# Optimization experiments

Hardware: AMD Instinct MI355X
Metric: run time of the kernel (lower is better)

The kernel has to match this reference:

```python
import jax, jax.numpy as jnp
import numpy as np

B, P, C = 2, 512, 21          # images, proposals/image, classes (incl background)
REG = 5                       # xc, yc, w, h, angle(deg)
DET = 100                     # detections_per_img
IMW, IMH = 1024, 800
SCORE_THRESH = 0.05
NMS_THR = 0.5
WEIGHTS = (10.0, 10.0, 5.0, 5.0, 3.0)
BBOX_XFORM_CLIP = float(np.log(1000.0 / 16.0))
MAXV = 8                      # max vertices of quad-quad intersection


def setup_inputs() -> dict:
    key = jax.random.key(0)
    k1, k2, k3 = jax.random.split(key, 3)
    class_logits = jax.random.normal(k1, (B * P, C), jnp.float32)
    box_regression = jax.random.normal(k2, (B * P, C * REG), jnp.float32)
    u = jax.random.uniform(k3, (B * P, 5), jnp.float32)
    rrects = jnp.stack([
        u[:, 0] * IMW,            # xc
        u[:, 1] * IMH,            # yc
        u[:, 2] * 200.0 + 16.0,   # w
        u[:, 3] * 200.0 + 16.0,   # h
        u[:, 4] * 360.0 - 180.0,  # angle in degrees
    ], axis=1)
    return {"class_logits": class_logits, "box_regression": box_regression, "rrects": rrects}


def rect_pts(r):
    # r [..., 5] -> corner points [..., 4, 2] (CCW quad in math coords)
    xc, yc, w, h, ang = (r[..., i] for i in range(5))
    t = ang * (jnp.pi / 180.0)
    c, s = jnp.cos(t), jnp.sin(t)
    dx, dy = w * 0.5, h * 0.5
    ox = jnp.stack([-dx, dx, dx, -dx], -1)
    oy = jnp.stack([-dy, -dy, dy, dy], -1)
    x = xc[..., None] + c[..., None] * ox - s[..., None] * oy
    y = yc[..., None] + s[..., None] * ox + c[..., None] * oy
    return jnp.stack([x, y], -1)


def decode(deltas, anchors):
    # BoxCoder.decode for rotated boxes, weights (wx,wy,ww,wh,wa)
    d = deltas.reshape(-1, C, REG) / jnp.asarray(WEIGHTS, deltas.dtype)
    dx, dy, dw, dh, da = (d[..., i] for i in range(REG))
    dw = jnp.minimum(dw, BBOX_XFORM_CLIP)
    dh = jnp.minimum(dh, BBOX_XFORM_CLIP)
    xc, yc, w, h, a = (anchors[:, i:i + 1] for i in range(5))
    px = dx * w + xc
    py = dy * h + yc
    pw = jnp.exp(dw) * w
    ph = jnp.exp(dh) * h
    pa = da * (180.0 / jnp.pi) + a
    return jnp.stack([px, py, pw, ph, pa], -1)  # [N, C, 5]


def _clip_edge(poly, n, a, b):
    # Sutherland-Hodgman clip of convex poly (buffer [MAXV,2], count n) by halfplane left of a->b
    d = b - a
    out = jnp.zeros((MAXV, 2), poly.dtype)
    m = jnp.int32(0)
    nn = jnp.maximum(n, 1)
    for i in range(MAXV):
        act = i < n
        s = poly[i]
        e = poly[jnp.mod(i + 1, nn)]
        cs = d[0] * (s[1] - a[1]) - d[1] * (s[0] - a[0])
        ce = d[0] * (e[1] - a[1]) - d[1] * (e[0] - a[0])
        denom = cs - ce
        t = cs / jnp.where(jnp.abs(denom) > 1e-12, denom, 1e-12)
        ip = s + t * (e - s)
        s_in = cs >= 0
        e_in = ce >= 0
        app1 = act & (s_in != e_in)           # crossing -> intersection point
        out = out.at[m].set(jnp.where(app1, ip, out[m]))
        m = m + app1.astype(jnp.int32)
        app2 = act & e_in                     # end point inside -> keep it
        out = out.at[m].set(jnp.where(app2, e, out[m]))
        m = m + app2.astype(jnp.int32)
    return out, m


def inter_area(p1, p2):
    # exact intersection area of two convex quads [4,2]
    poly = jnp.zeros((MAXV, 2), p1.dtype).at[:4].set(p1)
    n = jnp.int32(4)
    for k in range(4):
        poly, n = _clip_edge(poly, n, p2[k], p2[(k + 1) % 4])
    idx = jnp.arange(MAXV)
    nn = jnp.maximum(n, 1)
    nxt = jnp.mod(idx + 1, nn)
    cross = poly[:, 0] * poly[nxt, 1] - poly[nxt, 0] * poly[:, 1]
    area = 0.5 * jnp.abs(jnp.sum(jnp.where(idx < n, cross, 0.0)))
    return jnp.where(n >= 3, area, 0.0)


def _nms_one(args):
    # greedy rotated NMS on one (image,class) score-sorted set
    rr, valid = args                       # [P,5], [P] bool (sorted by desc score)
    pts = rect_pts(rr)                     # [P,4,2]
    areas = rr[:, 2] * rr[:, 3]
    inter = jax.vmap(lambda p: jax.vmap(lambda q: inter_area(p, q))(pts))(pts)
    iou = inter / (areas[:, None] + areas[None, :] - inter + 1e-8)
    n = rr.shape[0]
    def body(i, keep):
        sup = jnp.any(keep & (iou[i] > NMS_THR))
        return keep.at[i].set(valid[i] & jnp.logical_not(sup))
    return jax.lax.fori_loop(0, n, body, jnp.zeros((n,), bool))


def reference(class_logits, box_regression, rrects):
    scores = jax.nn.softmax(class_logits, -1)           # [N,C]
    proposals = decode(box_regression, rrects)          # [N,C,5]
    pts = rect_pts(proposals)                           # [N,C,4,2]
    mn, mx = pts.min(-2), pts.max(-2)
    bb = jnp.concatenate([mn, mx], -1)                  # xyxy [N,C,4]
    bb = jnp.stack([
        jnp.clip(bb[..., 0], 0.0, IMW - 1.0),
        jnp.clip(bb[..., 1], 0.0, IMH - 1.0),
        jnp.clip(bb[..., 2], 0.0, IMW - 1.0),
        jnp.clip(bb[..., 3], 0.0, IMH - 1.0),
    ], -1)

    # per-image, foreground classes only; [B, C-1, P, ...]
    sc = scores.reshape(B, P, C)[:, :, 1:].transpose(0, 2, 1)
    pr = proposals.reshape(B, P, C, 5)[:, :, 1:].transpose(0, 2, 1, 3)
    bx = bb.reshape(B, P, C, 4)[:, :, 1:].transpose(0, 2, 1, 3)

    valid = sc > SCORE_THRESH
    masked = jnp.where(valid, sc, -1.0)
    order = jnp.argsort(-masked, axis=-1)               # desc score per class
    sc_s = jnp.take_along_axis(masked, order, -1)
    valid_s = jnp.take_along_axis(valid, order, -1)
    pr_s = jnp.take_along_axis(pr, order[..., None], 2)
    bx_s = jnp.take_along_axis(bx, order[..., None], 2)

    keep = jax.lax.map(_nms_one, (jax.lax.stop_gradient(pr_s).reshape(-1, P, 5),
                                  valid_s.reshape(-1, P))).reshape(B, C - 1, P)
    keep = jax.lax.stop_gradient(keep)

    msk = jnp.where(keep, sc_s, -1.0)
    flat_s = msk.reshape(B, -1)                         # [B,(C-1)*P]
    top_idx = jax.lax.top_k(flat_s, DET)[1]
    sel_s = jnp.take_along_axis(flat_s, top_idx, -1)
    ok = sel_s > 0.0
    sel_bb = jnp.take_along_axis(bx_s.reshape(B, -1, 4), top_idx[..., None], 1)
    sel_rr = jnp.take_along_axis(pr_s.reshape(B, -1, 5), top_idx[..., None], 1)
    lab = jnp.broadcast_to(jnp.arange(1, C, dtype=jnp.int32)[:, None], (C - 1, P)).reshape(-1)
    sel_lab = lab[top_idx]

    out_bb = jnp.where(ok[..., None], sel_bb, 0.0)
    out_rr = jnp.where(ok[..., None], sel_rr, 0.0)
    out_sc = jnp.where(ok, sel_s, 0.0)
    out_lab = jnp.where(ok, sel_lab, 0)
    return out_bb, out_rr, out_sc, out_lab
```

## Files before the change

kernel.cpp:

```cpp
#include <hip/hip_runtime.h>
#include <stdint.h>

#pragma clang fp contract(off)

#define B_ 2
#define P_ 512
#define C_ 21
#define CF 20
#define DET 100
#define SCORE_THRESH 0.05f
#define NMS_THR 0.5f
#define BBOX_CLIP 4.135166556742356f
#define NC (CF * DET)

typedef unsigned long long u64;
typedef unsigned int u32;

__device__ __forceinline__ u32 f2o(float f) {
  u32 u = __float_as_uint(f);
  return (u & 0x80000000u) ? ~u : (u | 0x80000000u);
}
__device__ __forceinline__ float o2f(u32 o) {
  u32 u = (o & 0x80000000u) ? (o ^ 0x80000000u) : ~o;
  return __uint_as_float(u);
}

__global__ void __launch_bounds__(256)
prep_kernel(const float* __restrict__ logits,
            const float* __restrict__ breg,
            const float* __restrict__ rrects,
            float* __restrict__ scsS,
            float* __restrict__ ptsS,
            float* __restrict__ aabbS,
            float* __restrict__ pr5S,
            float* __restrict__ areaS,
            int* __restrict__ gV,
            u64* __restrict__ sup) {
  int g = blockIdx.x;
  int b = g / CF, cf = g % CF, c = cf + 1;
  int tid = threadIdx.x;

  __shared__ u64 lkey[P_];
  __shared__ int cnt;
  if (tid == 0) cnt = 0;

  u64 kreg[2];
  float fx[2][4], fy[2][4];
  float fab[2][4];
  float fp5[2][5];
  float far_[2];
  float fsc[2];
  #pragma unroll
  for (int e = 0; e < 2; ++e) {
    int p = tid + e * 256;
    int n = b * P_ + p;
    const float* lg = logits + n * C_;
    float mx = lg[0];
    for (int k = 1; k < C_; ++k) mx = fmaxf(mx, lg[k]);
    float den = 0.f;
    for (int k = 0; k < C_; ++k) den += expf(lg[k] - mx);
    float sc = expf(lg[c] - mx) / den;

    const float* d = breg + n * (C_ * 5) + c * 5;
    float dx = d[0] / 10.0f, dy = d[1] / 10.0f;
    float dw = d[2] / 5.0f, dh = d[3] / 5.0f, da = d[4] / 3.0f;
    dw = fminf(dw, BBOX_CLIP);
    dh = fminf(dh, BBOX_CLIP);
    const float* an = rrects + n * 5;
    float px = dx * an[2] + an[0];
    float py = dy * an[3] + an[1];
    float pw = expf(dw) * an[2];
    float ph = expf(dh) * an[3];
    float pa = da * 57.29577951308232f + an[4];
    fp5[e][0] = px; fp5[e][1] = py; fp5[e][2] = pw; fp5[e][3] = ph; fp5[e][4] = pa;
    far_[e] = pw * ph;

    float t = pa * 0.017453292519943295f;
    float cs = cosf(t), sn = sinf(t);
    float hx = pw * 0.5f, hy = ph * 0.5f;
    float ox[4] = {-hx, hx, hx, -hx};
    float oy[4] = {-hy, -hy, hy, hy};
    float minx = 1e30f, miny = 1e30f, maxx = -1e30f, maxy = -1e30f;
    #pragma unroll
    for (int qq = 0; qq < 4; ++qq) {
      float x = px + cs * ox[qq] - sn * oy[qq];
      float y = py + sn * ox[qq] + cs * oy[qq];
      fx[e][qq] = x; fy[e][qq] = y;
      minx = fminf(minx, x); maxx = fmaxf(maxx, x);
      miny = fminf(miny, y); maxy = fmaxf(maxy, y);
    }
    fab[e][0] = minx; fab[e][1] = miny; fab[e][2] = maxx; fab[e][3] = maxy;

    bool valid = sc > SCORE_THRESH;
    float v = valid ? sc : -1.0f;
    fsc[e] = v;
    u64 key = ((u64)f2o(v) << 32) | (u32)(~(u32)p);
    lkey[p] = key;
    kreg[e] = key;
    u64 m = __ballot(valid);
    if ((tid & 63) == 0) atomicAdd(&cnt, __popcll(m));
  }
  for (int w = tid; w < P_ * 8; w += 256) sup[(size_t)g * P_ * 8 + w] = 0ull;
  __syncthreads();

  u64 k0 = kreg[0], k1 = kreg[1];
  int r0 = 0, r1 = 0;
  for (int s = 0; s < P_; ++s) {
    u64 ks = lkey[s];
    r0 += (ks > k0) ? 1 : 0;
    r1 += (ks > k1) ? 1 : 0;
  }
  #pragma unroll
  for (int e = 0; e < 2; ++e) {
    if (fsc[e] > 0.f) {
      int r = (e == 0) ? r0 : r1;
      int so = g * P_ + r;
      scsS[so] = fsc[e];
      ((float4*)ptsS)[so * 2]     = make_float4(fx[e][0], fx[e][1], fx[e][2], fx[e][3]);
      ((float4*)ptsS)[so * 2 + 1] = make_float4(fy[e][0], fy[e][1], fy[e][2], fy[e][3]);
      ((float4*)aabbS)[so] = make_float4(fab[e][0], fab[e][1], fab[e][2], fab[e][3]);
      pr5S[so * 5 + 0] = fp5[e][0]; pr5S[so * 5 + 1] = fp5[e][1];
      pr5S[so * 5 + 2] = fp5[e][2]; pr5S[so * 5 + 3] = fp5[e][3];
      pr5S[so * 5 + 4] = fp5[e][4];
      areaS[so] = far_[e];
    }
  }
  if (tid == 0) gV[g] = cnt;
}

__device__ __forceinline__ float inter_area_reg(const float qx[4], const float qy[4],
                                                const float rx[4], const float ry[4]) {
  float px_[8], py_[8];
  #pragma unroll
  for (int t = 0; t < 8; ++t) { px_[t] = (t < 4) ? qx[t] : 0.f; py_[t] = (t < 4) ? qy[t] : 0.f; }
  int n = 4;
  #pragma unroll
  for (int e = 0; e < 4; ++e) {
    float a0 = rx[e], a1 = ry[e];
    float b0 = rx[(e + 1) & 3], b1 = ry[(e + 1) & 3];
    float dx = b0 - a0, dy = b1 - a1;
    float ox_[8], oy_[8];
    #pragma unroll
    for (int t = 0; t < 8; ++t) { ox_[t] = 0.f; oy_[t] = 0.f; }
    float cr[8];
    #pragma unroll
    for (int t = 0; t < 8; ++t) cr[t] = dx * (py_[t] - a1) - dy * (px_[t] - a0);
    int m = 0;
    int nn = (n > 1) ? n : 1;
    #pragma unroll
    for (int t = 0; t < 8; ++t) {
      bool act = t < n;
      float sx = px_[t], sy = py_[t];
      float ex, ey, ce;
      if (t == 7) { ex = px_[0]; ey = py_[0]; ce = cr[0]; }
      else {
        bool wrap = (t + 1 == nn);
        ex = wrap ? px_[0] : px_[t + 1];
        ey = wrap ? py_[0] : py_[t + 1];
        ce = wrap ? cr[0] : cr[t + 1];
      }
      float cs = cr[t];
      float denom = cs - ce;
      float dn = (fabsf(denom) > 1e-12f) ? denom : 1e-12f;
      float tt = cs / dn;
      float ipx = sx + tt * (ex - sx);
      float ipy = sy + tt * (ey - sy);
      bool s_in = cs >= 0.f, e_in = ce >= 0.f;
      bool app1 = act && (s_in != e_in);
      #pragma unroll
      for (int s2 = 0; s2 < 8; ++s2) {
        bool wr = app1 && (m == s2);
        ox_[s2] = wr ? ipx : ox_[s2];
        oy_[s2] = wr ? ipy : oy_[s2];
      }
      m += app1 ? 1 : 0;
      bool app2 = act && e_in;
      #pragma unroll
      for (int s2 = 0; s2 < 8; ++s2) {
        bool wr = app2 && (m == s2);
        ox_[s2] = wr ? ex : ox_[s2];
        oy_[s2] = wr ? ey : oy_[s2];
      }
      m += app2 ? 1 : 0;
    }
    n = m;
    #pragma unroll
    for (int t = 0; t < 8; ++t) { px_[t] = ox_[t]; py_[t] = oy_[t]; }
  }
  int nn = (n > 1) ? n : 1;
  float s = 0.f;
  #pragma unroll
  for (int t = 0; t < 8; ++t) {
    if (t < n) {
      float nx_x, nx_y;
      if (t == 7) { nx_x = px_[0]; nx_y = py_[0]; }
      else {
        bool wrap = (t + 1 == nn);
        nx_x = wrap ? px_[0] : px_[t + 1];
        nx_y = wrap ? py_[0] : py_[t + 1];
      }
      s += px_[t] * nx_y - nx_x * py_[t];
    }
  }
  float area = 0.5f * fabsf(s);
  return (n >= 3) ? area : 0.f;
}

#define PPT 4
#define TPB 256
__global__ void pair_kernel(const int* __restrict__ gV,
                            const float* __restrict__ aabbS,
                            const float* __restrict__ areaS,
                            const float* __restrict__ ptsS,
                            u64* __restrict__ sup) {
  int g = blockIdx.y;
  int V = gV[g];
  int Tp = V * (V - 1) / 2;
  int base = blockIdx.x * (TPB * PPT);
  if (base >= Tp) return;
  __shared__ u32 q[TPB * PPT];
  __shared__ int qn;
  int tid = threadIdx.x;
  if (tid == 0) qn = 0;
  __syncthreads();
  const float4* ab = (const float4*)aabbS;
  for (int t = 0; t < PPT; ++t) {
    int kk = base + t * TPB + tid;
    if (kk >= Tp) break;
    float kf = (float)kk;
    int i = (int)((1.0f + sqrtf(1.0f + 8.0f * kf)) * 0.5f);
    while (i * (i - 1) / 2 > kk) --i;
    while ((i + 1) * i / 2 <= kk) ++i;
    int j = kk - i * (i - 1) / 2;
    float4 bi = ab[g * P_ + i];
    float4 bj = ab[g * P_ + j];
    bool ov = (bi.x <= bj.z) && (bj.x <= bi.z) && (bi.y <= bj.w) && (bj.y <= bi.w);
    if (ov) {
      int s = atomicAdd(&qn, 1);
      q[s] = (u32)((i << 9) | j);
    }
  }
  __syncthreads();
  int nq = qn;
  const float4* pS = (const float4*)ptsS;
  for (int s = tid; s < nq; s += TPB) {
    u32 pk = q[s];
    int i = (int)(pk >> 9), j = (int)(pk & 511);
    float4 ax = pS[(g * P_ + i) * 2];
    float4 ay = pS[(g * P_ + i) * 2 + 1];
    float4 bx = pS[(g * P_ + j) * 2];
    float4 by = pS[(g * P_ + j) * 2 + 1];
    float qx[4] = {ax.x, ax.y, ax.z, ax.w};
    float qy[4] = {ay.x, ay.y, ay.z, ay.w};
    float rx[4] = {bx.x, bx.y, bx.z, bx.w};
    float ry[4] = {by.x, by.y, by.z, by.w};
    float ai = areaS[g * P_ + i];
    float aj = areaS[g * P_ + j];
    float inter = inter_area_reg(qx, qy, rx, ry);
    float iou = inter / (((ai + aj) - inter) + 1e-8f);
    if (iou > NMS_THR)
      atomicOr(&sup[((size_t)g * P_ + i) * 8 + (j >> 6)], 1ull << (j & 63));
  }
}

__global__ void greedy_kernel(const float* __restrict__ scsS, const int* __restrict__ gV,
                              const float* __restrict__ aabbS, const float* __restrict__ pr5S,
                              const u64* __restrict__ sup,
                              u64* __restrict__ cand, float* __restrict__ rec) {
  int g = blockIdx.x;
  int tid = threadIdx.x;
  __shared__ u64 lsup[P_ * 8];
  __shared__ u32 skeep[16];
  int V = gV[g];
  for (int w = tid; w < V * 8; w += 64) lsup[w] = sup[(size_t)g * P_ * 8 + w];
  __syncthreads();
  u64 keepw = 0;
  u64 cur = (tid < 8 && V > 0) ? lsup[tid] : 0ull;
  for (int i = 0; i < V; ++i) {
    u64 nxt = (tid < 8 && (i + 1) < V) ? lsup[(i + 1) * 8 + tid] : 0ull;
    bool supd = __any((cur & keepw) != 0ull);
    if (!supd && tid == (i >> 6)) keepw |= 1ull << (i & 63);
    cur = nxt;
  }
  if (tid < 8) { skeep[tid * 2] = (u32)keepw; skeep[tid * 2 + 1] = (u32)(keepw >> 32); }
  __syncthreads();
  int cls = g % CF;
  int tot = 0;
  #pragma unroll
  for (int t = 0; t < 16; ++t) tot += __popc(skeep[t]);
  for (int r = tid; r < V; r += 64) {
    if ((skeep[r >> 5] >> (r & 31)) & 1u) {
      int slot = __popc(skeep[r >> 5] & ((1u << (r & 31)) - 1u));
      for (int t = 0; t < (r >> 5); ++t) slot += __popc(skeep[t]);
      if (slot < DET) {
        float sv = scsS[g * P_ + r];
        int flat = cls * P_ + r;
        cand[g * DET + slot] = ((u64)f2o(sv) << 32) | (u32)(~(u32)flat);
        int so = g * P_ + r;
        float* rr = rec + (size_t)(g * DET + slot) * 12;
        rr[0] = fminf(fmaxf(aabbS[so * 4 + 0], 0.f), 1023.0f);
        rr[1] = fminf(fmaxf(aabbS[so * 4 + 1], 0.f), 799.0f);
        rr[2] = fminf(fmaxf(aabbS[so * 4 + 2], 0.f), 1023.0f);
        rr[3] = fminf(fmaxf(aabbS[so * 4 + 3], 0.f), 799.0f);
        rr[4] = pr5S[so * 5 + 0]; rr[5] = pr5S[so * 5 + 1]; rr[6] = pr5S[so * 5 + 2];
        rr[7] = pr5S[so * 5 + 3]; rr[8] = pr5S[so * 5 + 4];
        rr[9] = sv;
        rr[10] = (float)(cls + 1);
        rr[11] = 0.f;
      }
    }
  }
  int fill = tot < DET ? tot : DET;
  for (int s = fill + tid; s < DET; s += 64) cand[g * DET + s] = 0ull;
}

__global__ void rank_kernel(const u64* __restrict__ cand, const float* __restrict__ rec,
                            float* __restrict__ out) {
  int b = blockIdx.y;
  int tid = threadIdx.x;
  __shared__ u64 lc[NC];
  __shared__ int ncand;
  if (tid == 0) ncand = 0;
  __syncthreads();
  int nz = 0;
  for (int i = tid; i < NC; i += 256) {
    u64 v = cand[b * NC + i];
    lc[i] = v;
    nz += (v != 0ull) ? 1 : 0;
  }
  u64 m = __ballot(nz > 0);
  if (nz > 0) atomicAdd(&ncand, nz);
  (void)m;
  __syncthreads();
  int ci = blockIdx.x * 256 + tid;
  if (ci >= NC) return;
  if (blockIdx.x == 0 && tid < DET && tid >= ncand) {
    int o_bb = (b * DET + tid) * 4;
    int o_rr = B_ * DET * 4 + (b * DET + tid) * 5;
    int o_sc = B_ * DET * 9 + b * DET + tid;
    int o_lab = B_ * DET * 10 + b * DET + tid;
    out[o_bb + 0] = 0.f; out[o_bb + 1] = 0.f; out[o_bb + 2] = 0.f; out[o_bb + 3] = 0.f;
    out[o_rr + 0] = 0.f; out[o_rr + 1] = 0.f; out[o_rr + 2] = 0.f;
    out[o_rr + 3] = 0.f; out[o_rr + 4] = 0.f;
    out[o_sc] = 0.f;
    out[o_lab] = 0.f;
  }
  u64 k = lc[ci];
  if (k == 0ull) return;
  int rank = 0;
  #pragma unroll
  for (int gp = 0; gp < CF; ++gp) {
    int lo = 0, hi = DET;
    while (lo < hi) {
      int mid = (lo + hi) >> 1;
      if (lc[gp * DET + mid] > k) lo = mid + 1; else hi = mid;
    }
    rank += lo;
  }
  if (rank >= DET) return;
  const float* rr = rec + (size_t)(b * NC + ci) * 12;
  int o_bb = (b * DET + rank) * 4;
  int o_rr = B_ * DET * 4 + (b * DET + rank) * 5;
  int o_sc = B_ * DET * 9 + b * DET + rank;
  int o_lab = B_ * DET * 10 + b * DET + rank;
  out[o_bb + 0] = rr[0]; out[o_bb + 1] = rr[1];
  out[o_bb + 2] = rr[2]; out[o_bb + 3] = rr[3];
  out[o_rr + 0] = rr[4]; out[o_rr + 1] = rr[5]; out[o_rr + 2] = rr[6];
  out[o_rr + 3] = rr[7]; out[o_rr + 4] = rr[8];
  out[o_sc] = rr[9];
  out[o_lab] = rr[10];
}

extern "C" void kernel_launch(void* const* d_in, const int* in_sizes, int n_in,
                              void* d_out, int out_size, void* d_ws, size_t ws_size,
                              hipStream_t stream) {
  const float* logits = (const float*)d_in[0];
  const float* breg   = (const float*)d_in[1];
  const float* rrects = (const float*)d_in[2];
  float* out = (float*)d_out;

  const int G = B_ * CF;
  u64*   sup  = (u64*)d_ws;
  u64*   cand = sup + (size_t)G * P_ * 8;
  int*   gV   = (int*)(cand + G * DET);
  float* scsS = (float*)(gV + 64);
  float* ptsS = scsS + (size_t)G * P_;
  float* aabbS = ptsS + (size_t)G * P_ * 8;
  float* pr5S = aabbS + (size_t)G * P_ * 4;
  float* areaS = pr5S + (size_t)G * P_ * 5;
  float* rec  = areaS + (size_t)G * P_;

  prep_kernel<<<G, 256, 0, stream>>>(logits, breg, rrects,
                                     scsS, ptsS, aabbS, pr5S, areaS, gV, sup);
  pair_kernel<<<dim3(128, G), TPB, 0, stream>>>(gV, aabbS, areaS, ptsS, sup);
  greedy_kernel<<<G, 64, 0, stream>>>(scsS, gV, aabbS, pr5S, sup, cand, rec);
  rank_kernel<<<dim3((NC + 255) / 256, B_), 256, 0, stream>>>(cand, rec, out);
}
```

Measured before the change: 133.8 us.

## Compact valid keys before ranking and use one proposal per thread in prep

The prep kernel now runs 512 threads per (image,class) group, one proposal each, instead of 256 threads handling two. Valid keys are compacted into shared memory with a ballot prefix sum, so each thread ranks itself only against the valid candidates rather than all 512, unrolled by four. The logits loads and softmax loop are fully unrolled into registers. This cuts the O(P^2) rank loop when few scores pass the threshold, at the cost of more registers per thread and an extra barrier.

```diff
diff --git a/kernel.cpp b/kernel.cpp
--- a/kernel.cpp
+++ b/kernel.cpp
@@ -25,7 +25,7 @@
   return __uint_as_float(u);
 }
 
-__global__ void __launch_bounds__(256)
+__global__ void __launch_bounds__(512)
 prep_kernel(const float* __restrict__ logits,
             const float* __restrict__ breg,
             const float* __restrict__ rrects,
@@ -39,93 +39,102 @@
   int g = blockIdx.x;
   int b = g / CF, cf = g % CF, c = cf + 1;
   int tid = threadIdx.x;
-
-  __shared__ u64 lkey[P_];
-  __shared__ int cnt;
-  if (tid == 0) cnt = 0;
-
-  u64 kreg[2];
-  float fx[2][4], fy[2][4];
-  float fab[2][4];
-  float fp5[2][5];
-  float far_[2];
-  float fsc[2];
-  #pragma unroll
-  for (int e = 0; e < 2; ++e) {
-    int p = tid + e * 256;
-    int n = b * P_ + p;
-    const float* lg = logits + n * C_;
-    float mx = lg[0];
-    for (int k = 1; k < C_; ++k) mx = fmaxf(mx, lg[k]);
-    float den = 0.f;
-    for (int k = 0; k < C_; ++k) den += expf(lg[k] - mx);
-    float sc = expf(lg[c] - mx) / den;
-
-    const float* d = breg + n * (C_ * 5) + c * 5;
-    float dx = d[0] / 10.0f, dy = d[1] / 10.0f;
-    float dw = d[2] / 5.0f, dh = d[3] / 5.0f, da = d[4] / 3.0f;
-    dw = fminf(dw, BBOX_CLIP);
-    dh = fminf(dh, BBOX_CLIP);
-    const float* an = rrects + n * 5;
-    float px = dx * an[2] + an[0];
-    float py = dy * an[3] + an[1];
-    float pw = expf(dw) * an[2];
-    float ph = expf(dh) * an[3];
-    float pa = da * 57.29577951308232f + an[4];
-    fp5[e][0] = px; fp5[e][1] = py; fp5[e][2] = pw; fp5[e][3] = ph; fp5[e][4] = pa;
-    far_[e] = pw * ph;
-
-    float t = pa * 0.017453292519943295f;
-    float cs = cosf(t), sn = sinf(t);
-    float hx = pw * 0.5f, hy = ph * 0.5f;
-    float ox[4] = {-hx, hx, hx, -hx};
-    float oy[4] = {-hy, -hy, hy, hy};
-    float minx = 1e30f, miny = 1e30f, maxx = -1e30f, maxy = -1e30f;
-    #pragma unroll
-    for (int qq = 0; qq < 4; ++qq) {
-      float x = px + cs * ox[qq] - sn * oy[qq];
-      float y = py + sn * ox[qq] + cs * oy[qq];
-      fx[e][qq] = x; fy[e][qq] = y;
-      minx = fminf(minx, x); maxx = fmaxf(maxx, x);
-      miny = fminf(miny, y); maxy = fmaxf(maxy, y);
-    }
-    fab[e][0] = minx; fab[e][1] = miny; fab[e][2] = maxx; fab[e][3] = maxy;
-
-    bool valid = sc > SCORE_THRESH;
-    float v = valid ? sc : -1.0f;
-    fsc[e] = v;
-    u64 key = ((u64)f2o(v) << 32) | (u32)(~(u32)p);
-    lkey[p] = key;
-    kreg[e] = key;
-    u64 m = __ballot(valid);
-    if ((tid & 63) == 0) atomicAdd(&cnt, __popcll(m));
-  }
-  for (int w = tid; w < P_ * 8; w += 256) sup[(size_t)g * P_ * 8 + w] = 0ull;
-  __syncthreads();
-
-  u64 k0 = kreg[0], k1 = kreg[1];
-  int r0 = 0, r1 = 0;
-  for (int s = 0; s < P_; ++s) {
-    u64 ks = lkey[s];
-    r0 += (ks > k0) ? 1 : 0;
-    r1 += (ks > k1) ? 1 : 0;
-  }
-  #pragma unroll
-  for (int e = 0; e < 2; ++e) {
-    if (fsc[e] > 0.f) {
-      int r = (e == 0) ? r0 : r1;
-      int so = g * P_ + r;
-      scsS[so] = fsc[e];
-      ((float4*)ptsS)[so * 2]     = make_float4(fx[e][0], fx[e][1], fx[e][2], fx[e][3]);
-      ((float4*)ptsS)[so * 2 + 1] = make_float4(fy[e][0], fy[e][1], fy[e][2], fy[e][3]);
-      ((float4*)aabbS)[so] = make_float4(fab[e][0], fab[e][1], fab[e][2], fab[e][3]);
-      pr5S[so * 5 + 0] = fp5[e][0]; pr5S[so * 5 + 1] = fp5[e][1];
-      pr5S[so * 5 + 2] = fp5[e][2]; pr5S[so * 5 + 3] = fp5[e][3];
-      pr5S[so * 5 + 4] = fp5[e][4];
-      areaS[so] = far_[e];
-    }
-  }
-  if (tid == 0) gV[g] = cnt;
+  int w = tid >> 6, lane = tid & 63;
+
+  __shared__ u64 ckey[P_ + 8];
+  __shared__ int wcnt[8];
+
+  int p = tid;
+  int n = b * P_ + p;
+  const float* lgp = logits + n * C_;
+  float lg[C_];
+  #pragma unroll
+  for (int k = 0; k < C_; ++k) lg[k] = lgp[k];
+  float mx = lg[0];
+  #pragma unroll
+  for (int k = 1; k < C_; ++k) mx = fmaxf(mx, lg[k]);
+  float den = 0.f, num = 0.f;
+  #pragma unroll
+  for (int k = 0; k < C_; ++k) {
+    float ex = expf(lg[k] - mx);
+    den += ex;
+    num = (k == c) ? ex : num;
+  }
+  float sc = num / den;
+
+  const float* d = breg + n * (C_ * 5) + c * 5;
+  float dx = d[0] / 10.0f, dy = d[1] / 10.0f;
+  float dw = d[2] / 5.0f, dh = d[3] / 5.0f, da = d[4] / 3.0f;
+  dw = fminf(dw, BBOX_CLIP);
+  dh = fminf(dh, BBOX_CLIP);
+  const float* an = rrects + n * 5;
+  float px = dx * an[2] + an[0];
+  float py = dy * an[3] + an[1];
+  float pw = expf(dw) * an[2];
+  float ph = expf(dh) * an[3];
+  float pa = da * 57.29577951308232f + an[4];
+  float area = pw * ph;
+
+  float t = pa * 0.017453292519943295f;
+  float cs = cosf(t), sn = sinf(t);
+  float hx = pw * 0.5f, hy = ph * 0.5f;
+  float ox[4] = {-hx, hx, hx, -hx};
+  float oy[4] = {-hy, -hy, hy, hy};
+  float X[4], Y[4];
+  float minx = 1e30f, miny = 1e30f, maxx = -1e30f, maxy = -1e30f;
+  #pragma unroll
+  for (int q = 0; q < 4; ++q) {
+    float x = px + cs * ox[q] - sn * oy[q];
+    float y = py + sn * ox[q] + cs * oy[q];
+    X[q] = x; Y[q] = y;
+    minx = fminf(minx, x); maxx = fmaxf(maxx, x);
+    miny = fminf(miny, y); maxy = fmaxf(maxy, y);
+  }
+
+  bool valid = sc > SCORE_THRESH;
+  float v = valid ? sc : -1.0f;
+  u64 key = ((u64)f2o(v) << 32) | (u32)(~(u32)p);
+
+  u64 m = __ballot(valid);
+  if (lane == 0) wcnt[w] = __popcll(m);
+
+  for (int z = tid; z < P_ * 8; z += 512) sup[(size_t)g * P_ * 8 + z] = 0ull;
+  __syncthreads();
+
+  int V = 0, myb = 0;
+  #pragma unroll
+  for (int si = 0; si < 8; ++si) {
+    int cnti = wcnt[si];
+    myb += (si < w) ? cnti : 0;
+    V += cnti;
+  }
+  int slot = myb + __popcll(m & ((1ull << lane) - 1ull));
+  if (valid) ckey[slot] = key;
+  if (tid < 8) ckey[V + tid] = 0ull;
+  __syncthreads();
+
+  int Vr = (V + 3) & ~3;
+  int r = 0;
+  for (int s = 0; s < Vr; s += 4) {
+    u64 a0 = ckey[s], a1 = ckey[s + 1], a2 = ckey[s + 2], a3 = ckey[s + 3];
+    r += (a0 > key) ? 1 : 0;
+    r += (a1 > key) ? 1 : 0;
+    r += (a2 > key) ? 1 : 0;
+    r += (a3 > key) ? 1 : 0;
+  }
+
+  if (valid) {
+    int so = g * P_ + r;
+    scsS[so] = v;
+    ((float4*)ptsS)[so * 2]     = make_float4(X[0], X[1], X[2], X[3]);
+    ((float4*)ptsS)[so * 2 + 1] = make_float4(Y[0], Y[1], Y[2], Y[3]);
+    ((float4*)aabbS)[so] = make_float4(minx, miny, maxx, maxy);
+    pr5S[so * 5 + 0] = px; pr5S[so * 5 + 1] = py;
+    pr5S[so * 5 + 2] = pw; pr5S[so * 5 + 3] = ph;
+    pr5S[so * 5 + 4] = pa;
+    areaS[so] = area;
+  }
+  if (tid == 0) gV[g] = V;
 }
 
 __device__ __forceinline__ float inter_area_reg(const float qx[4], const float qy[4],
@@ -390,7 +399,7 @@
   float* areaS = pr5S + (size_t)G * P_ * 5;
   float* rec  = areaS + (size_t)G * P_;
 
-  prep_kernel<<<G, 256, 0, stream>>>(logits, breg, rrects,
+  prep_kernel<<<G, 512, 0, stream>>>(logits, breg, rrects,
                                      scsS, ptsS, aabbS, pr5S, areaS, gV, sup);
   pair_kernel<<<dim3(128, G), TPB, 0, stream>>>(gV, aabbS, areaS, ptsS, sup);
   greedy_kernel<<<G, 64, 0, stream>>>(scsS, gV, aabbS, pr5S, sup, cand, rec);
```

Result: faster. 129.0 us (-3.6%).
